# Kernel tuning notes

Measured on AMD Instinct MI355X. Metric: run time of the kernel, lower is better.

The kernel has to match this reference:

```python
import jax, jax.numpy as jnp
import numpy as np

N, E, IN = 50000, 800000, 64
HC, FC1, FC2, FC3, OUT = 96, 256, 128, 64, 8
EPS = 1e-5


def setup_inputs() -> dict:
    key = jax.random.key(0)
    ks = jax.random.split(key, 24)
    def lin(k, fi, fo):
        # kaiming_uniform with relu gain: bound = sqrt(6/fi)
        b = np.sqrt(6.0 / fi)
        return jax.random.uniform(k, (fi, fo), jnp.float32, -b, b)
    inp = {
        'x': jax.random.normal(ks[0], (N, IN), jnp.float32),
        'edge_index': jax.random.randint(ks[1], (2, E), 0, N, jnp.int64),
        'w1': lin(ks[2], IN, HC), 'b1': jnp.zeros((HC,), jnp.float32),
        'g1': jax.random.uniform(ks[3], (HC,), jnp.float32, 0.5, 1.5), 'be1': jax.random.normal(ks[4], (HC,), jnp.float32) * 0.1,
        'w2': lin(ks[5], HC, HC), 'b2': jnp.zeros((HC,), jnp.float32),
        'g2': jax.random.uniform(ks[6], (HC,), jnp.float32, 0.5, 1.5), 'be2': jax.random.normal(ks[7], (HC,), jnp.float32) * 0.1,
        'w3': lin(ks[8], HC, HC), 'b3': jnp.zeros((HC,), jnp.float32),
        'g3': jax.random.uniform(ks[9], (HC,), jnp.float32, 0.5, 1.5), 'be3': jax.random.normal(ks[10], (HC,), jnp.float32) * 0.1,
        'lw1': lin(ks[11], HC, FC1), 'lb1': jnp.zeros((FC1,), jnp.float32),
        'lw2': lin(ks[12], FC1, FC2), 'lb2': jnp.zeros((FC2,), jnp.float32),
        'lw3': lin(ks[13], FC2, FC3), 'lb3': jnp.zeros((FC3,), jnp.float32),
        'lw4': lin(ks[14], FC3, OUT), 'lb4': jnp.zeros((OUT,), jnp.float32),
    }
    return inp


def _gcn(x, w, b, src, dst, norm):
    # GCNConv: out[dst] += norm_e * (x @ w)[src]; then + bias
    h = x @ w
    msg = h[src] * norm[:, None]
    return jax.ops.segment_sum(msg, dst, num_segments=N) + b


def _bn_eval(x, g, be):
    # eval-mode BatchNorm1d with running_mean=0, running_var=1
    return x / jnp.sqrt(1.0 + EPS) * g + be


def reference(x, edge_index, w1, b1, g1, be1, w2, b2, g2, be2, w3, b3, g3, be3,
              lw1, lb1, lw2, lb2, lw3, lb3, lw4, lb4):
    loops = jnp.arange(N, dtype=edge_index.dtype)
    src = jnp.concatenate([edge_index[0], loops])
    dst = jnp.concatenate([edge_index[1], loops])
    deg = jax.ops.segment_sum(jnp.ones_like(src, jnp.float32), dst, num_segments=N)
    dinv = jax.lax.rsqrt(deg)  # deg >= 1 due to self loops
    norm = dinv[src] * dinv[dst]

    h = jax.nn.relu(_bn_eval(_gcn(x, w1, b1, src, dst, norm), g1, be1))
    h = jax.nn.relu(_bn_eval(_gcn(h, w2, b2, src, dst, norm), g2, be2))
    h = jax.nn.relu(_bn_eval(_gcn(h, w3, b3, src, dst, norm), g3, be3))
    h = jax.nn.relu(h @ lw1 + lb1)
    h = jax.nn.relu(h @ lw2 + lb2)
    h = jax.nn.relu(h @ lw3 + lb3)
    return h @ lw4 + lb4
```

## Files before the change

### kernel.cpp

```cpp
#include <hip/hip_runtime.h>


#define GN 50000
#define GE 800000
#define NPART 98
#define PSLOT 9216
#define CHK 2048

typedef __attribute__((ext_vector_type(8))) short bf16x8;
typedef __attribute__((ext_vector_type(4))) float floatx4;
typedef __attribute__((ext_vector_type(2))) float floatx2;
typedef __attribute__((ext_vector_type(4))) unsigned int uintx4;

__device__ __forceinline__ float ar1_b2f(unsigned short h) {
    return __uint_as_float(((unsigned)h) << 16);
}
__device__ __forceinline__ unsigned short ar1_f2b(float f) {
    unsigned u = __float_as_uint(f);
    u = u + 0x7FFFu + ((u >> 16) & 1u);
    return (unsigned short)(u >> 16);
}
__device__ __forceinline__ floatx2 ar1_up2(unsigned w) {
    floatx2 t;
    t[0] = __uint_as_float(w << 16);
    t[1] = __uint_as_float(w & 0xFFFF0000u);
    return t;
}

__device__ __forceinline__ int ar1_det64(const int* ei) {
    int l = (int)threadIdx.x & 63;
    int nz = 0;
#pragma unroll
    for (int k = 0; k < 4; k++)
        nz += (ei[2 * (l + 64 * k) + 1] != 0) ? 1 : 0;
#pragma unroll
    for (int o = 1; o < 64; o <<= 1)
        nz += __shfl_xor(nz, o, 64);
    return (nz < 8) ? 1 : 0;
}
__device__ __forceinline__ int ar1_detf32(const unsigned short* xw) {
    int l = (int)threadIdx.x & 63;
    int c = 0;
#pragma unroll
    for (int k = 0; k < 4; k++) {
        unsigned short w = xw[2 * (l + 64 * k)];
        int ex = (w >> 7) & 0xFF;
        if (w == 0 || (ex >= 90 && ex <= 150)) c++;
    }
#pragma unroll
    for (int o = 1; o < 64; o <<= 1)
        c += __shfl_xor(c, o, 64);
    return (c > 200) ? 0 : 1;
}

struct PackAll {
    const void* src[7];
    unsigned short* dst[7];
    int K[7], M[7], start[8];
};
struct SmallCvt {
    const void* src[4];
    float* dst[4];
    int n[4];
    const void* gb[9];
    float* ss[6];
};

__global__ __launch_bounds__(256)
void Arthur1_16458314678864_kernel(PackAll pa, SmallCvt sc,
                                   const int* __restrict__ ei,
                                   const unsigned short* __restrict__ xw,
                                   int* flagI, int* flagF,
                                   int* __restrict__ gcur,
                                   unsigned int* __restrict__ pairs,
                                   unsigned short* __restrict__ xb,
                                   unsigned short* __restrict__ bufA,
                                   unsigned short* __restrict__ bufB,
                                   float* __restrict__ dinvp) {
    int b = (int)blockIdx.x;
    int tid = (int)threadIdx.x;
    if (b < 391) {
        __shared__ int cnt[NPART], base[NPART], cur[NPART];
        for (int i = tid; i < NPART; i += 256) { cnt[i] = 0; cur[i] = 0; }
        int is64 = ar1_det64(ei);
        __syncthreads();
        int e0 = b * CHK;
        unsigned pk[8]; int q[8];
#pragma unroll
        for (int k = 0; k < 8; k++) {
            int e = e0 + k * 256 + tid;
            q[k] = -1; pk[k] = 0;
            if (e < GE) {
                int s = is64 ? ei[2 * e] : ei[e];
                int d = is64 ? ei[2 * (GE + e)] : ei[GE + e];
                if ((unsigned)s < (unsigned)GN && (unsigned)d < (unsigned)GN) {
                    int qq = d >> 9;
                    q[k] = qq;
                    pk[k] = (unsigned)s | ((unsigned)(d & 511) << 17);
                    atomicAdd(&cnt[qq], 1);
                }
            }
        }
        __syncthreads();
        for (int i = tid; i < NPART; i += 256)
            base[i] = (cnt[i] > 0) ? atomicAdd(&gcur[i], cnt[i]) : 0;
        __syncthreads();
#pragma unroll
        for (int k = 0; k < 8; k++) {
            if (q[k] >= 0) {
                int r = base[q[k]] + atomicAdd(&cur[q[k]], 1);
                if (r < PSLOT) pairs[(size_t)q[k] * PSLOT + r] = pk[k];
            }
        }
    } else if (b < 436) {
        int f = ar1_detf32(xw);
        int frag_g = (b - 391) * 4 + (tid >> 6);
        if (frag_g >= 178) return;
        int w = 0;
        while (w < 6 && frag_g >= pa.start[w + 1]) w++;
        int frag = frag_g - pa.start[w];
        int K = pa.K[w], M = pa.M[w];
        int lane = tid & 63;
        int nch = K >> 5;
        int t = frag / nch, c = frag - t * nch;
        int n = t * 16 + (lane & 15);
        int k0 = c * 32 + (lane >> 4) * 8;
        unsigned short* o = pa.dst[w] + ((size_t)frag * 64 + lane) * 8;
        for (int j = 0; j < 8; j++) {
            unsigned short v = 0;
            if (n < M) {
                int idx = (k0 + j) * M + n;
                v = f ? ar1_f2b(((const float*)pa.src[w])[idx])
                      : ((const unsigned short*)pa.src[w])[idx];
            }
            o[j] = v;
        }
    } else if (b == 436) {
        int f = ar1_detf32(xw);
        int i64 = ar1_det64(ei);
        if (tid == 0) { flagI[0] = i64; flagF[0] = f; dinvp[GN] = 0.f; }
        if (tid < 96) {
            bufA[(size_t)GN * 96 + tid] = 0;
            bufB[(size_t)GN * 96 + tid] = 0;
        }
        if (tid >= 96 && tid < 160) xb[(size_t)GN * 64 + (tid - 96)] = 0;
        const float C = 0.9999950000374997f;
        for (int s = 0; s < 4; s++) {
            for (int i = tid; i < sc.n[s]; i += 256) {
                float v = f ? ((const float*)sc.src[s])[i]
                            : ar1_b2f(((const unsigned short*)sc.src[s])[i]);
                sc.dst[s][i] = v;
            }
        }
        for (int k = 0; k < 3; k++) {
            for (int i = tid; i < 96; i += 256) {
                float bb, g, be;
                if (f) {
                    bb = ((const float*)sc.gb[3 * k + 0])[i];
                    g  = ((const float*)sc.gb[3 * k + 1])[i];
                    be = ((const float*)sc.gb[3 * k + 2])[i];
                } else {
                    bb = ar1_b2f(((const unsigned short*)sc.gb[3 * k + 0])[i]);
                    g  = ar1_b2f(((const unsigned short*)sc.gb[3 * k + 1])[i]);
                    be = ar1_b2f(((const unsigned short*)sc.gb[3 * k + 2])[i]);
                }
                sc.ss[2 * k + 0][i] = C * g;
                sc.ss[2 * k + 1][i] = bb * C * g + be;
            }
        }
    } else {
        int f = ar1_detf32(xw);
        size_t t = (size_t)(b - 437) * 256 + (size_t)tid;
        size_t i0 = t * 8;
        if (i0 < (size_t)GN * 64) {
            bf16x8 o;
            if (f) {
                const float* xf = (const float*)xw;
                floatx4 a = *((const floatx4*)(xf + i0));
                floatx4 c = *((const floatx4*)(xf + i0 + 4));
#pragma unroll
                for (int j = 0; j < 4; j++) {
                    o[j]     = (short)ar1_f2b(a[j]);
                    o[4 + j] = (short)ar1_f2b(c[j]);
                }
            } else {
                o = *((const bf16x8*)(xw + i0));
            }
            *((bf16x8*)(xb + i0)) = o;
        }
    }
}

__global__ __launch_bounds__(256)
void ar1_csr(const unsigned int* __restrict__ pairs, const int* __restrict__ gcur,
             int* __restrict__ csr, int* __restrict__ indeg,
             int* __restrict__ offs, float* __restrict__ dinv,
             unsigned short* __restrict__ xb) {
    __shared__ int ncnt[512], pre[512], cur[512], psum[16], red[256];
    int p = (int)blockIdx.x, tid = (int)threadIdx.x;
    red[tid] = (tid < p && tid < NPART) ? gcur[tid] : 0;
    __syncthreads();
    for (int o = 128; o > 0; o >>= 1) {
        if (tid < o) red[tid] += red[tid + o];
        __syncthreads();
    }
    int gbase = red[0];
    int cntE = gcur[p];
    if (cntE > PSLOT) cntE = PSLOT;
    for (int i = tid; i < 512; i += 256) ncnt[i] = 0;
    __syncthreads();
    const unsigned int* pp = pairs + (size_t)p * PSLOT;
    for (int i = tid; i < cntE; i += 256) atomicAdd(&ncnt[pp[i] >> 17], 1);
    __syncthreads();
    if (tid < 16) {
        int s = 0;
        for (int j = tid * 32; j < tid * 32 + 32; j++) { pre[j] = s; s += ncnt[j]; }
        psum[tid] = s;
    }
    __syncthreads();
    if (tid == 0) {
        int s = 0;
        for (int j = 0; j < 16; j++) { int t = psum[j]; psum[j] = s; s += t; }
    }
    __syncthreads();
    if (tid < 16)
        for (int j = tid * 32; j < tid * 32 + 32; j++) pre[j] += psum[tid];
    __syncthreads();
    for (int j = tid; j < 512; j += 256) {
        cur[j] = pre[j];
        int node = p * 512 + j;
        if (node < GN) {
            indeg[node] = ncnt[j];
            offs[node] = gbase + pre[j];
            dinv[node] = rsqrtf((float)(ncnt[j] + 1));
        }
    }
    __syncthreads();
    for (int i = tid; i < cntE; i += 256) {
        unsigned v = pp[i];
        int r = atomicAdd(&cur[v >> 17], 1);
        csr[gbase + r] = (int)(v & 0x1FFFFu);
    }
    for (int i = tid; i < 512 * 8; i += 256) {
        int j = i >> 3, c = i & 7;
        int node = p * 512 + j;
        if (node < GN) {
            float sc = rsqrtf((float)(ncnt[j] + 1));
            bf16x8 v = *((bf16x8*)(xb + (size_t)node * 64 + c * 8));
#pragma unroll
            for (int jj = 0; jj < 8; jj++)
                v[jj] = (short)ar1_f2b(sc * ar1_b2f((unsigned short)v[jj]));
            *((bf16x8*)(xb + (size_t)node * 64 + c * 8)) = v;
        }
    }
}

__global__ __launch_bounds__(256, 8)
void ar1_gat64(const unsigned short* __restrict__ Xb, const int* __restrict__ offs,
               const int* __restrict__ indeg, const int* __restrict__ csr,
               const float* __restrict__ dinv,
               unsigned short* __restrict__ Agg) {
    int tid = (int)threadIdx.x, wv = tid >> 6, lane = tid & 63;
    int node = (int)blockIdx.x * 4 + wv;
    int chunk = lane & 7, eslot = lane >> 3;
    float di = dinv[node];
    int off = offs[node], cnt = indeg[node];

    floatx2 acc2[4];
#pragma unroll
    for (int d = 0; d < 4; d++) acc2[d] = (floatx2){0.f, 0.f};

    for (int base = 0; base < cnt; base += 16) {
        int ss[2];
#pragma unroll
        for (int k = 0; k < 2; k++) {
            int e = base + k * 8 + eslot;
            ss[k] = (e < cnt) ? csr[off + e] : GN;
        }
        uintx4 hh[2];
#pragma unroll
        for (int k = 0; k < 2; k++)
            hh[k] = *((const uintx4*)(Xb + (size_t)ss[k] * 64 + chunk * 8));
#pragma unroll
        for (int k = 0; k < 2; k++)
#pragma unroll
            for (int d = 0; d < 4; d++)
                acc2[d] += ar1_up2(hh[k][d]);
    }
#pragma unroll
    for (int d = 0; d < 4; d++)
#pragma unroll
        for (int c = 0; c < 2; c++) {
            acc2[d][c] += __shfl_xor(acc2[d][c], 8, 64);
            acc2[d][c] += __shfl_xor(acc2[d][c], 16, 64);
            acc2[d][c] += __shfl_xor(acc2[d][c], 32, 64);
        }
    if (eslot == 0) {
        bf16x8 h = *((const bf16x8*)(Xb + (size_t)node * 64 + chunk * 8));
        bf16x8 o;
#pragma unroll
        for (int j = 0; j < 8; j++)
            o[j] = (short)ar1_f2b(di * (acc2[j >> 1][j & 1] +
                                        ar1_b2f((unsigned short)h[j])));
        *((bf16x8*)(Agg + (size_t)node * 64 + chunk * 8)) = o;
    }
}

__global__ __launch_bounds__(256, 8)
void ar1_gat96(const unsigned short* __restrict__ H, const int* __restrict__ offs,
               const int* __restrict__ indeg, const int* __restrict__ csr,
               const float* __restrict__ dinv,
               unsigned short* __restrict__ Agg) {
    int tid = (int)threadIdx.x, wv = tid >> 6, lane = tid & 63;
    int node = (int)blockIdx.x * 4 + wv;
    int chunk = lane % 12, eslot = lane / 12;
    float di = dinv[node];
    int off = offs[node], cnt = indeg[node];

    floatx2 acc2[4];
#pragma unroll
    for (int d = 0; d < 4; d++) acc2[d] = (floatx2){0.f, 0.f};

    if (lane < 48) {
        for (int base = 0; base < cnt; base += 16) {
            int ss[4];
#pragma unroll
            for (int k = 0; k < 4; k++) {
                int e = base + k * 4 + eslot;
                ss[k] = (e < cnt) ? csr[off + e] : GN;
            }
            uintx4 hh[4];
#pragma unroll
            for (int k = 0; k < 4; k++)
                hh[k] = *((const uintx4*)(H + (size_t)ss[k] * 96 + chunk * 8));
#pragma unroll
            for (int k = 0; k < 4; k++)
#pragma unroll
                for (int d = 0; d < 4; d++)
                    acc2[d] += ar1_up2(hh[k][d]);
        }
    }
#pragma unroll
    for (int d = 0; d < 4; d++)
#pragma unroll
        for (int c = 0; c < 2; c++) {
            float a1 = __shfl(acc2[d][c], lane + 12, 64);
            float a2 = __shfl(acc2[d][c], lane + 24, 64);
            float a3 = __shfl(acc2[d][c], lane + 36, 64);
            acc2[d][c] += a1 + a2 + a3;
        }
    if (lane < 12) {
        bf16x8 hs = *((const bf16x8*)(H + (size_t)node * 96 + chunk * 8));
        bf16x8 o;
#pragma unroll
        for (int j = 0; j < 8; j++)
            o[j] = (short)ar1_f2b(di * (acc2[j >> 1][j & 1] +
                                        ar1_b2f((unsigned short)hs[j])));
        *((bf16x8*)(Agg + (size_t)node * 96 + chunk * 8)) = o;
    }
}

__global__ __launch_bounds__(512, 8)
void ar1_gem1(const unsigned int* __restrict__ Agg, const float* __restrict__ dinv,
              const unsigned short* __restrict__ Bp,
              const float* __restrict__ scale, const float* __restrict__ shift,
              unsigned short* __restrict__ C) {
    __shared__ unsigned short AL[16 * 72];
    int tid = (int)threadIdx.x;
    int nb = (int)blockIdx.x * 16;
    {
        int row = tid >> 5, dw = tid & 31;
        ((unsigned*)AL)[row * 36 + dw] = Agg[(size_t)nb * 32 + tid];
    }
    __syncthreads();

    int wv = tid >> 6, lane = tid & 63;
    if (wv < 6) {
        int m = lane & 15, quad = lane >> 4, t = wv;
        floatx4 g = (floatx4){0.f, 0.f, 0.f, 0.f};
#pragma unroll
        for (int c = 0; c < 2; c++) {
            bf16x8 a = *((const bf16x8*)(AL + (size_t)m * 72 + c * 32 + quad * 8));
            bf16x8 bfr = *((const bf16x8*)(Bp + ((size_t)(t * 2 + c) * 64 + lane) * 8));
            g = __builtin_amdgcn_mfma_f32_16x16x32_bf16(a, bfr, g, 0, 0, 0);
        }
#pragma unroll
        for (int r = 0; r < 4; r++) {
            int row = nb + quad * 4 + r;
            int col = t * 16 + m;
            float v = g[r] * scale[col] + shift[col];
            C[(size_t)row * 96 + col] = ar1_f2b(dinv[row] * fmaxf(v, 0.f));
        }
    }
}

__global__ __launch_bounds__(512, 8)
void ar1_gem2(const unsigned int* __restrict__ Agg, const float* __restrict__ dinv,
              const unsigned short* __restrict__ Bp,
              const float* __restrict__ scale, const float* __restrict__ shift,
              unsigned short* __restrict__ C) {
    __shared__ unsigned short AL[16 * 104];
    int tid = (int)threadIdx.x;
    int nb = (int)blockIdx.x * 16;
    for (int i = tid; i < 768; i += 512) {
        int row = i / 48, dw = i - row * 48;
        ((unsigned*)AL)[row * 52 + dw] = Agg[(size_t)nb * 48 + i];
    }
    __syncthreads();

    int wv = tid >> 6, lane = tid & 63;
    if (wv < 6) {
        int m = lane & 15, quad = lane >> 4, t = wv;
        floatx4 g = (floatx4){0.f, 0.f, 0.f, 0.f};
#pragma unroll
        for (int c = 0; c < 3; c++) {
            bf16x8 a = *((const bf16x8*)(AL + (size_t)m * 104 + c * 32 + quad * 8));
            bf16x8 bfr = *((const bf16x8*)(Bp + ((size_t)(t * 3 + c) * 64 + lane) * 8));
            g = __builtin_amdgcn_mfma_f32_16x16x32_bf16(a, bfr, g, 0, 0, 0);
        }
#pragma unroll
        for (int r = 0; r < 4; r++) {
            int row = nb + quad * 4 + r;
            int col = t * 16 + m;
            float v = g[r] * scale[col] + shift[col];
            C[(size_t)row * 96 + col] = ar1_f2b(dinv[row] * fmaxf(v, 0.f));
        }
    }
}

__global__ __launch_bounds__(1024, 8)
void ar1_mlp(const unsigned int* __restrict__ Agg,
             const unsigned short* __restrict__ b2w,
             const float* __restrict__ sc3, const float* __restrict__ sh3,
             const unsigned short* __restrict__ b3,
             const unsigned short* __restrict__ b4,
             const unsigned short* __restrict__ b5,
             const unsigned short* __restrict__ b6,
             const float* __restrict__ lb0, const float* __restrict__ lb1,
             const float* __restrict__ lb2, const float* __restrict__ lb3,
             void* __restrict__ out, const int* __restrict__ f32out) {
    __shared__ unsigned short AL[16 * 104];
    __shared__ unsigned short H0[16 * 104];
    __shared__ unsigned short H1[16 * 264];
    __shared__ unsigned short H2[16 * 136];
    __shared__ unsigned short H3[16 * 72];
    int tid = (int)threadIdx.x, wv = tid >> 6, lane = tid & 63;
    int nb = (int)blockIdx.x * 16;
    int m = lane & 15, quad = lane >> 4;

    if (tid < 768) {
        int row = tid / 48, dw = tid - row * 48;
        ((unsigned*)AL)[row * 52 + dw] = Agg[(size_t)nb * 48 + tid];
    }
    __syncthreads();

    if (wv < 6) {
        int t = wv;
        floatx4 g = (floatx4){0.f, 0.f, 0.f, 0.f};
#pragma unroll
        for (int c = 0; c < 3; c++) {
            bf16x8 a = *((const bf16x8*)(AL + (size_t)m * 104 + c * 32 + quad * 8));
            bf16x8 bfr = *((const bf16x8*)(b2w + ((size_t)(t * 3 + c) * 64 + lane) * 8));
            g = __builtin_amdgcn_mfma_f32_16x16x32_bf16(a, bfr, g, 0, 0, 0);
        }
#pragma unroll
        for (int r = 0; r < 4; r++) {
            int col = t * 16 + m;
            float v = g[r] * sc3[col] + sh3[col];
            H0[(quad * 4 + r) * 104 + col] = ar1_f2b(fmaxf(v, 0.f));
        }
    }
    __syncthreads();

    {
        int t = wv;
        floatx4 g = (floatx4){0.f, 0.f, 0.f, 0.f};
#pragma unroll
        for (int c = 0; c < 3; c++) {
            bf16x8 a = *((const bf16x8*)(H0 + (size_t)m * 104 + c * 32 + quad * 8));
            bf16x8 bfr = *((const bf16x8*)(b3 + ((size_t)(t * 3 + c) * 64 + lane) * 8));
            g = __builtin_amdgcn_mfma_f32_16x16x32_bf16(a, bfr, g, 0, 0, 0);
        }
#pragma unroll
        for (int r = 0; r < 4; r++) {
            int col = t * 16 + m;
            H1[(quad * 4 + r) * 264 + col] = ar1_f2b(fmaxf(g[r] + lb0[col], 0.f));
        }
    }
    __syncthreads();

    if (wv < 8) {
        int t = wv;
        floatx4 g = (floatx4){0.f, 0.f, 0.f, 0.f};
#pragma unroll
        for (int c = 0; c < 8; c++) {
            bf16x8 a = *((const bf16x8*)(H1 + (size_t)m * 264 + c * 32 + quad * 8));
            bf16x8 bfr = *((const bf16x8*)(b4 + ((size_t)(t * 8 + c) * 64 + lane) * 8));
            g = __builtin_amdgcn_mfma_f32_16x16x32_bf16(a, bfr, g, 0, 0, 0);
        }
#pragma unroll
        for (int r = 0; r < 4; r++) {
            int col = t * 16 + m;
            H2[(quad * 4 + r) * 136 + col] = ar1_f2b(fmaxf(g[r] + lb1[col], 0.f));
        }
    }
    __syncthreads();

    if (wv < 4) {
        int t = wv;
        floatx4 g = (floatx4){0.f, 0.f, 0.f, 0.f};
#pragma unroll
        for (int c = 0; c < 4; c++) {
            bf16x8 a = *((const bf16x8*)(H2 + (size_t)m * 136 + c * 32 + quad * 8));
            bf16x8 bfr = *((const bf16x8*)(b5 + ((size_t)(t * 4 + c) * 64 + lane) * 8));
            g = __builtin_amdgcn_mfma_f32_16x16x32_bf16(a, bfr, g, 0, 0, 0);
        }
#pragma unroll
        for (int r = 0; r < 4; r++) {
            int col = t * 16 + m;
            H3[(quad * 4 + r) * 72 + col] = ar1_f2b(fmaxf(g[r] + lb2[col], 0.f));
        }
    }
    __syncthreads();

    if (wv == 0) {
        floatx4 g = (floatx4){0.f, 0.f, 0.f, 0.f};
#pragma unroll
        for (int c = 0; c < 2; c++) {
            bf16x8 a = *((const bf16x8*)(H3 + (size_t)m * 72 + c * 32 + quad * 8));
            bf16x8 bfr = *((const bf16x8*)(b6 + ((size_t)c * 64 + lane) * 8));
            g = __builtin_amdgcn_mfma_f32_16x16x32_bf16(a, bfr, g, 0, 0, 0);
        }
        int wf32 = f32out[0];
#pragma unroll
        for (int r = 0; r < 4; r++) {
            int row = nb + quad * 4 + r;
            if (m < 8) {
                float v = g[r] + lb3[m];
                if (wf32) ((float*)out)[(size_t)row * 8 + m] = v;
                else ((unsigned short*)out)[(size_t)row * 8 + m] = ar1_f2b(v);
            }
        }
    }
}

extern "C" void kernel_launch(void* const* d_in, const int* in_sizes, int n_in,
                              void* d_out, int out_size, void* d_ws, size_t ws_size,
                              hipStream_t stream) {
    (void)in_sizes; (void)n_in; (void)out_size;

    char* p = (char*)d_ws;
    unsigned short* bufA = (unsigned short*)p; p += (size_t)(GN + 1) * 96 * 2;
    unsigned short* bufB = (unsigned short*)p; p += (size_t)(GN + 1) * 96 * 2;
    unsigned short* xb   = (unsigned short*)p; p += (size_t)(GN + 1) * 64 * 2;
    unsigned short* agg64 = (unsigned short*)p; p += (size_t)GN * 64 * 2;
    unsigned short* agg96 = (unsigned short*)p; p += (size_t)GN * 96 * 2;
    unsigned int* pairs = (unsigned int*)p; p += (size_t)NPART * PSLOT * 4;
    int* indeg  = (int*)p;    p += (size_t)GN * 4;
    int* offs   = (int*)p;    p += (size_t)GN * 4;
    float* dinv = (float*)p;  p += (size_t)GN * 4 + 64;
    int* csr    = (int*)p;    p += (size_t)GE * 4;
    int* gcur   = (int*)p;    p += 1024;
    int* flagI  = (int*)p;    p += 1024;
    int* flagF  = (int*)p;    p += 1024;
    unsigned short* bpArena = (unsigned short*)p; p += 91136 * 2;
    float* fArena = (float*)p; p += 2048 * 4;
    size_t need = (size_t)(p - (char*)d_ws);
    if (ws_size < need) {
        hipMemsetAsync(d_out, 0x41, (size_t)GN * 8 * 2, stream);
        return;
    }

    unsigned short* bp[7];
    int bpn[7] = {6144, 9216, 9216, 24576, 32768, 8192, 1024};
    {
        unsigned short* q = bpArena;
        for (int i = 0; i < 7; i++) { bp[i] = q; q += bpn[i]; }
    }

    float* lb[4]; float* ss[6];
    {
        float* q = fArena;
        int ln[4] = {256, 128, 64, 8};
        for (int i = 0; i < 4; i++) { lb[i] = q; q += ln[i]; }
        for (int i = 0; i < 6; i++) { ss[i] = q; q += 96; }
    }

    const int* ei = (const int*)d_in[1];
    const unsigned short* xw = (const unsigned short*)d_in[0];

    hipMemsetAsync(gcur, 0, NPART * 4, stream);
    {
        PackAll pa;
        int wsrc[7] = {2, 6, 10, 14, 16, 18, 20};
        int Ks[7] = {64, 96, 96, 96, 256, 128, 64};
        int Ms[7] = {96, 96, 96, 256, 128, 64, 8};
        int cum = 0;
        for (int i = 0; i < 7; i++) {
            pa.src[i] = d_in[wsrc[i]]; pa.dst[i] = bp[i];
            pa.K[i] = Ks[i]; pa.M[i] = Ms[i];
            pa.start[i] = cum;
            cum += (Ms[i] + 15) / 16 * (Ks[i] / 32);
        }
        pa.start[7] = cum;
        SmallCvt sc;
        int lsrc[4] = {15, 17, 19, 21};
        int ln[4] = {256, 128, 64, 8};
        for (int i = 0; i < 4; i++) { sc.src[i] = d_in[lsrc[i]]; sc.dst[i] = lb[i]; sc.n[i] = ln[i]; }
        int gsrc[9] = {3, 4, 5, 7, 8, 9, 11, 12, 13};
        for (int i = 0; i < 9; i++) sc.gb[i] = d_in[gsrc[i]];
        for (int i = 0; i < 6; i++) sc.ss[i] = ss[i];
        Arthur1_16458314678864_kernel<<<2000, 256, 0, stream>>>(
            pa, sc, ei, xw, flagI, flagF, gcur, pairs, xb, bufA, bufB, dinv);
    }
    ar1_csr<<<NPART, 256, 0, stream>>>(pairs, gcur, csr, indeg, offs, dinv, xb);

    const int GB = GN / 4;
    const int CB = GN / 16;

    ar1_gat64<<<GB, 256, 0, stream>>>(xb, offs, indeg, csr, dinv, agg64);
    ar1_gem1<<<CB, 512, 0, stream>>>((const unsigned*)agg64, dinv,
                                     bp[0], ss[0], ss[1], bufA);
    ar1_gat96<<<GB, 256, 0, stream>>>(bufA, offs, indeg, csr, dinv, agg96);
    ar1_gem2<<<CB, 512, 0, stream>>>((const unsigned*)agg96, dinv,
                                     bp[1], ss[2], ss[3], bufB);
    ar1_gat96<<<GB, 256, 0, stream>>>(bufB, offs, indeg, csr, dinv, agg96);
    ar1_mlp<<<CB, 1024, 0, stream>>>((const unsigned*)agg96,
                                     bp[2], ss[4], ss[5],
                                     bp[3], bp[4], bp[5], bp[6],
                                     lb[0], lb[1], lb[2], lb[3], d_out, flagF);
}
```

Before: 277.4 us.

## Quantize hidden GCN activations to uint8 with per-row scale for gathers

The GEMM epilogues now quantize each post-ReLU 96-wide row to unsigned 8-bit values with a per-row float scale stored in a 128-byte padded row. A new gather kernel dequantizes neighbor rows while aggregating, so the bytes read per edge drop from 192. The cost is quantization error in layers 2 and 3, an extra scale load per neighbor, and an LDS staging step plus a row-max reduction in the GEMMs.

```diff
diff --git a/kernel.cpp b/kernel.cpp
--- a/kernel.cpp
+++ b/kernel.cpp
@@ -74,8 +74,8 @@
                                    int* __restrict__ gcur,
                                    unsigned int* __restrict__ pairs,
                                    unsigned short* __restrict__ xb,
-                                   unsigned short* __restrict__ bufA,
-                                   unsigned short* __restrict__ bufB,
+                                   unsigned char* __restrict__ bufA8,
+                                   unsigned char* __restrict__ bufB8,
                                    float* __restrict__ dinvp) {
     int b = (int)blockIdx.x;
     int tid = (int)threadIdx.x;
@@ -139,10 +139,8 @@
         int f = ar1_detf32(xw);
         int i64 = ar1_det64(ei);
         if (tid == 0) { flagI[0] = i64; flagF[0] = f; dinvp[GN] = 0.f; }
-        if (tid < 96) {
-            bufA[(size_t)GN * 96 + tid] = 0;
-            bufB[(size_t)GN * 96 + tid] = 0;
-        }
+        if (tid < 32) ((unsigned*)bufA8)[(size_t)GN * 32 + tid] = 0;
+        if (tid >= 32 && tid < 64) ((unsigned*)bufB8)[(size_t)GN * 32 + (tid - 32)] = 0;
         if (tid >= 96 && tid < 160) xb[(size_t)GN * 64 + (tid - 96)] = 0;
         const float C = 0.9999950000374997f;
         for (int s = 0; s < 4; s++) {
@@ -307,56 +305,61 @@
 }
 
 __global__ __launch_bounds__(256, 8)
-void ar1_gat96(const unsigned short* __restrict__ H, const int* __restrict__ offs,
-               const int* __restrict__ indeg, const int* __restrict__ csr,
-               const float* __restrict__ dinv,
-               unsigned short* __restrict__ Agg) {
+void ar1_gat96i8(const unsigned char* __restrict__ B8, const int* __restrict__ offs,
+                 const int* __restrict__ indeg, const int* __restrict__ csr,
+                 const float* __restrict__ dinv,
+                 unsigned short* __restrict__ Agg) {
     int tid = (int)threadIdx.x, wv = tid >> 6, lane = tid & 63;
     int node = (int)blockIdx.x * 4 + wv;
-    int chunk = lane % 12, eslot = lane / 12;
+    int chunk = lane & 7, eslot = lane >> 3;
     float di = dinv[node];
     int off = offs[node], cnt = indeg[node];
 
-    floatx2 acc2[4];
-#pragma unroll
-    for (int d = 0; d < 4; d++) acc2[d] = (floatx2){0.f, 0.f};
-
-    if (lane < 48) {
-        for (int base = 0; base < cnt; base += 16) {
-            int ss[4];
-#pragma unroll
-            for (int k = 0; k < 4; k++) {
-                int e = base + k * 4 + eslot;
-                ss[k] = (e < cnt) ? csr[off + e] : GN;
-            }
-            uintx4 hh[4];
-#pragma unroll
-            for (int k = 0; k < 4; k++)
-                hh[k] = *((const uintx4*)(H + (size_t)ss[k] * 96 + chunk * 8));
-#pragma unroll
-            for (int k = 0; k < 4; k++)
-#pragma unroll
-                for (int d = 0; d < 4; d++)
-                    acc2[d] += ar1_up2(hh[k][d]);
-        }
-    }
-#pragma unroll
-    for (int d = 0; d < 4; d++)
-#pragma unroll
-        for (int c = 0; c < 2; c++) {
-            float a1 = __shfl(acc2[d][c], lane + 12, 64);
-            float a2 = __shfl(acc2[d][c], lane + 24, 64);
-            float a3 = __shfl(acc2[d][c], lane + 36, 64);
-            acc2[d][c] += a1 + a2 + a3;
-        }
-    if (lane < 12) {
-        bf16x8 hs = *((const bf16x8*)(H + (size_t)node * 96 + chunk * 8));
-        bf16x8 o;
-#pragma unroll
-        for (int j = 0; j < 8; j++)
-            o[j] = (short)ar1_f2b(di * (acc2[j >> 1][j & 1] +
-                                        ar1_b2f((unsigned short)hs[j])));
-        *((bf16x8*)(Agg + (size_t)node * 96 + chunk * 8)) = o;
+    float acc[16];
+#pragma unroll
+    for (int j = 0; j < 16; j++) acc[j] = 0.f;
+
+    for (int base = 0; base < cnt; base += 16) {
+        int e0 = base + eslot, e1 = base + 8 + eslot;
+        int s0 = (e0 < cnt) ? csr[off + e0] : GN;
+        int s1 = (e1 < cnt) ? csr[off + e1] : GN;
+        const unsigned* r0 = (const unsigned*)(B8 + (size_t)s0 * 128);
+        const unsigned* r1 = (const unsigned*)(B8 + (size_t)s1 * 128);
+        uintx4 h0 = *((const uintx4*)(r0 + chunk * 4));
+        uintx4 h1 = *((const uintx4*)(r1 + chunk * 4));
+        float c0 = __uint_as_float(r0[24]);
+        float c1 = __uint_as_float(r1[24]);
+#pragma unroll
+        for (int d = 0; d < 4; d++)
+#pragma unroll
+            for (int bb = 0; bb < 4; bb++) {
+                acc[d * 4 + bb] += (float)((h0[d] >> (8 * bb)) & 0xFFu) * c0;
+                acc[d * 4 + bb] += (float)((h1[d] >> (8 * bb)) & 0xFFu) * c1;
+            }
+    }
+#pragma unroll
+    for (int j = 0; j < 16; j++) {
+        acc[j] += __shfl_xor(acc[j], 8, 64);
+        acc[j] += __shfl_xor(acc[j], 16, 64);
+        acc[j] += __shfl_xor(acc[j], 32, 64);
+    }
+    if (eslot == 0 && chunk < 6) {
+        const unsigned* rs = (const unsigned*)(B8 + (size_t)node * 128);
+        uintx4 hs = *((const uintx4*)(rs + chunk * 4));
+        float scs = __uint_as_float(rs[24]);
+        bf16x8 o0, o1;
+#pragma unroll
+        for (int d = 0; d < 4; d++)
+#pragma unroll
+            for (int bb = 0; bb < 4; bb++) {
+                int j = d * 4 + bb;
+                float v = di * (acc[j] +
+                                (float)((hs[d] >> (8 * bb)) & 0xFFu) * scs);
+                unsigned short w = ar1_f2b(v);
+                if (j < 8) o0[j] = (short)w; else o1[j - 8] = (short)w;
+            }
+        *((bf16x8*)(Agg + (size_t)node * 96 + chunk * 16)) = o0;
+        *((bf16x8*)(Agg + (size_t)node * 96 + chunk * 16 + 8)) = o1;
     }
 }
 
@@ -364,8 +367,9 @@
 void ar1_gem1(const unsigned int* __restrict__ Agg, const float* __restrict__ dinv,
               const unsigned short* __restrict__ Bp,
               const float* __restrict__ scale, const float* __restrict__ shift,
-              unsigned short* __restrict__ C) {
+              unsigned char* __restrict__ B8) {
     __shared__ unsigned short AL[16 * 72];
+    __shared__ float CT[16 * 96];
     int tid = (int)threadIdx.x;
     int nb = (int)blockIdx.x * 16;
     {
@@ -389,7 +393,34 @@
             int row = nb + quad * 4 + r;
             int col = t * 16 + m;
             float v = g[r] * scale[col] + shift[col];
-            C[(size_t)row * 96 + col] = ar1_f2b(dinv[row] * fmaxf(v, 0.f));
+            CT[(quad * 4 + r) * 96 + col] = dinv[row] * fmaxf(v, 0.f);
+        }
+    }
+    __syncthreads();
+
+#pragma unroll
+    for (int rr = 0; rr < 2; rr++) {
+        int row = wv + rr * 8;
+        floatx4 v = (floatx4){0.f, 0.f, 0.f, 0.f};
+        if (lane < 24) v = *((const floatx4*)(CT + row * 96 + lane * 4));
+        float mx = fmaxf(fmaxf(v[0], v[1]), fmaxf(v[2], v[3]));
+#pragma unroll
+        for (int o = 1; o < 64; o <<= 1)
+            mx = fmaxf(mx, __shfl_xor(mx, o, 64));
+        float inv = (mx > 0.f) ? 255.f / mx : 0.f;
+        if (lane < 32) {
+            unsigned q = 0;
+            if (lane < 24) {
+#pragma unroll
+                for (int i = 0; i < 4; i++) {
+                    int qi = (int)(v[i] * inv + 0.5f);
+                    qi = qi > 255 ? 255 : qi;
+                    q |= ((unsigned)qi) << (8 * i);
+                }
+            } else if (lane == 24) {
+                q = __float_as_uint(mx * (1.f / 255.f));
+            }
+            ((unsigned*)B8)[(size_t)(nb + row) * 32 + lane] = q;
         }
     }
 }
@@ -398,8 +429,9 @@
 void ar1_gem2(const unsigned int* __restrict__ Agg, const float* __restrict__ dinv,
               const unsigned short* __restrict__ Bp,
               const float* __restrict__ scale, const float* __restrict__ shift,
-              unsigned short* __restrict__ C) {
+              unsigned char* __restrict__ B8) {
     __shared__ unsigned short AL[16 * 104];
+    __shared__ float CT[16 * 96];
     int tid = (int)threadIdx.x;
     int nb = (int)blockIdx.x * 16;
     for (int i = tid; i < 768; i += 512) {
@@ -423,7 +455,34 @@
             int row = nb + quad * 4 + r;
             int col = t * 16 + m;
             float v = g[r] * scale[col] + shift[col];
-            C[(size_t)row * 96 + col] = ar1_f2b(dinv[row] * fmaxf(v, 0.f));
+            CT[(quad * 4 + r) * 96 + col] = dinv[row] * fmaxf(v, 0.f);
+        }
+    }
+    __syncthreads();
+
+#pragma unroll
+    for (int rr = 0; rr < 2; rr++) {
+        int row = wv + rr * 8;
+        floatx4 v = (floatx4){0.f, 0.f, 0.f, 0.f};
+        if (lane < 24) v = *((const floatx4*)(CT + row * 96 + lane * 4));
+        float mx = fmaxf(fmaxf(v[0], v[1]), fmaxf(v[2], v[3]));
+#pragma unroll
+        for (int o = 1; o < 64; o <<= 1)
+            mx = fmaxf(mx, __shfl_xor(mx, o, 64));
+        float inv = (mx > 0.f) ? 255.f / mx : 0.f;
+        if (lane < 32) {
+            unsigned q = 0;
+            if (lane < 24) {
+#pragma unroll
+                for (int i = 0; i < 4; i++) {
+                    int qi = (int)(v[i] * inv + 0.5f);
+                    qi = qi > 255 ? 255 : qi;
+                    q |= ((unsigned)qi) << (8 * i);
+                }
+            } else if (lane == 24) {
+                q = __float_as_uint(mx * (1.f / 255.f));
+            }
+            ((unsigned*)B8)[(size_t)(nb + row) * 32 + lane] = q;
         }
     }
 }
@@ -550,8 +609,8 @@
     (void)in_sizes; (void)n_in; (void)out_size;
 
     char* p = (char*)d_ws;
-    unsigned short* bufA = (unsigned short*)p; p += (size_t)(GN + 1) * 96 * 2;
-    unsigned short* bufB = (unsigned short*)p; p += (size_t)(GN + 1) * 96 * 2;
+    unsigned char* bufA8 = (unsigned char*)p; p += (size_t)(GN + 1) * 128;
+    unsigned char* bufB8 = (unsigned char*)p; p += (size_t)(GN + 1) * 128;
     unsigned short* xb   = (unsigned short*)p; p += (size_t)(GN + 1) * 64 * 2;
     unsigned short* agg64 = (unsigned short*)p; p += (size_t)GN * 64 * 2;
     unsigned short* agg96 = (unsigned short*)p; p += (size_t)GN * 96 * 2;
@@ -611,7 +670,7 @@
         for (int i = 0; i < 9; i++) sc.gb[i] = d_in[gsrc[i]];
         for (int i = 0; i < 6; i++) sc.ss[i] = ss[i];
         Arthur1_16458314678864_kernel<<<2000, 256, 0, stream>>>(
-            pa, sc, ei, xw, flagI, flagF, gcur, pairs, xb, bufA, bufB, dinv);
+            pa, sc, ei, xw, flagI, flagF, gcur, pairs, xb, bufA8, bufB8, dinv);
     }
     ar1_csr<<<NPART, 256, 0, stream>>>(pairs, gcur, csr, indeg, offs, dinv, xb);
 
@@ -620,11 +679,11 @@
 
     ar1_gat64<<<GB, 256, 0, stream>>>(xb, offs, indeg, csr, dinv, agg64);
     ar1_gem1<<<CB, 512, 0, stream>>>((const unsigned*)agg64, dinv,
-                                     bp[0], ss[0], ss[1], bufA);
-    ar1_gat96<<<GB, 256, 0, stream>>>(bufA, offs, indeg, csr, dinv, agg96);
+                                     bp[0], ss[0], ss[1], bufA8);
+    ar1_gat96i8<<<GB, 256, 0, stream>>>(bufA8, offs, indeg, csr, dinv, agg96);
     ar1_gem2<<<CB, 512, 0, stream>>>((const unsigned*)agg96, dinv,
-                                     bp[1], ss[2], ss[3], bufB);
-    ar1_gat96<<<GB, 256, 0, stream>>>(bufB, offs, indeg, csr, dinv, agg96);
+                                     bp[1], ss[2], ss[3], bufB8);
+    ar1_gat96i8<<<GB, 256, 0, stream>>>(bufB8, offs, indeg, csr, dinv, agg96);
     ar1_mlp<<<CB, 1024, 0, stream>>>((const unsigned*)agg96,
                                      bp[2], ss[4], ss[5],
                                      bp[3], bp[4], bp[5], bp[6],
```

Measured after the change: 287.7 us. +3.7%, slower.
